# Optimization experiments

Measured on AMD Instinct MI355X. Metric: run time of the kernel, lower is better.

## Reference

```python
import jax, jax.numpy as jnp
import numpy as np

B = 2
C = 256          # hidden_dim / d_model
NH = 8           # attention heads
NL = 4           # feature levels
NP = 4           # sampling points per head per level
DH = C // NH
FF = 1024
NLAYERS = 6
SHAPES = [(64, 64), (32, 32), (16, 16), (8, 8)]
CIN = 256
OUT_CH = 2
IMG = 256


def setup_inputs() -> dict:
    key = jax.random.key(0)
    ks = iter(jax.random.split(key, 64))

    def nrm(shape, s=0.02):
        return jax.random.normal(next(ks), shape, jnp.float32) * s

    inp = {}
    for i, (h, w) in enumerate(SHAPES):
        inp[f"f{i}"] = jax.random.normal(next(ks), (B, CIN, h, w), jnp.float32)
    # input_proj: 1x1 conv + GroupNorm per level
    inp["proj_w"] = nrm((NL, C, CIN))
    inp["proj_b"] = jnp.zeros((NL, C), jnp.float32)
    inp["gn_w"] = jnp.ones((NL, C), jnp.float32)
    inp["gn_b"] = jnp.zeros((NL, C), jnp.float32)
    inp["level_embed"] = nrm((NL, C), 1.0)
    # 6 encoder layers (stacked params)
    inp["so_w"] = nrm((NLAYERS, NH * NL * NP * 2, C))   # sampling offsets
    inp["so_b"] = nrm((NLAYERS, NH * NL * NP * 2), 0.1)
    inp["aw_w"] = nrm((NLAYERS, NH * NL * NP, C))       # attention weights
    inp["aw_b"] = jnp.zeros((NLAYERS, NH * NL * NP), jnp.float32)
    inp["vp_w"] = nrm((NLAYERS, C, C))                   # value proj
    inp["vp_b"] = jnp.zeros((NLAYERS, C), jnp.float32)
    inp["op_w"] = nrm((NLAYERS, C, C))                   # output proj
    inp["op_b"] = jnp.zeros((NLAYERS, C), jnp.float32)
    inp["n1_w"] = jnp.ones((NLAYERS, C), jnp.float32)
    inp["n1_b"] = jnp.zeros((NLAYERS, C), jnp.float32)
    inp["l1_w"] = nrm((NLAYERS, FF, C))
    inp["l1_b"] = jnp.zeros((NLAYERS, FF), jnp.float32)
    inp["l2_w"] = nrm((NLAYERS, C, FF))
    inp["l2_b"] = jnp.zeros((NLAYERS, C), jnp.float32)
    inp["n2_w"] = jnp.ones((NLAYERS, C), jnp.float32)
    inp["n2_b"] = jnp.zeros((NLAYERS, C), jnp.float32)
    # classifier head convs
    inp["c1_w"] = nrm((64, C, 3, 3))
    inp["c1_b"] = jnp.zeros((64,), jnp.float32)
    inp["c2_w"] = nrm((OUT_CH, 64, 3, 3))
    inp["c2_b"] = jnp.zeros((OUT_CH,), jnp.float32)
    return inp


def group_norm(x, w, b, groups=32, eps=1e-5):
    Bq, Cc, H, W = x.shape
    xg = x.reshape(Bq, groups, Cc // groups, H, W)
    mu = xg.mean((2, 3, 4), keepdims=True)
    var = xg.var((2, 3, 4), keepdims=True)
    xg = (xg - mu) * jax.lax.rsqrt(var + eps)
    return xg.reshape(Bq, Cc, H, W) * w[None, :, None, None] + b[None, :, None, None]


def layer_norm(x, w, b, eps=1e-5):
    mu = x.mean(-1, keepdims=True)
    var = x.var(-1, keepdims=True)
    return (x - mu) * jax.lax.rsqrt(var + eps) * w + b


def pos_embed_sine(h, w, num_feats=C // 2):
    # PositionEmbeddingSine(normalize=True), mask all-False -> cumsum of ones
    eps = 1e-6
    scale = 2.0 * np.pi
    y = (jnp.arange(1, h + 1, dtype=jnp.float32) / (h + eps)) * scale
    x = (jnp.arange(1, w + 1, dtype=jnp.float32) / (w + eps)) * scale
    dim_t = 10000.0 ** (2.0 * (jnp.arange(num_feats) // 2).astype(jnp.float32) / num_feats)

    def enc(v):
        p = v[:, None] / dim_t  # [n, num_feats]
        return jnp.stack([jnp.sin(p[:, 0::2]), jnp.cos(p[:, 1::2])], -1).reshape(v.shape[0], num_feats)

    pe_y = enc(y)  # [h, 128]
    pe_x = enc(x)  # [w, 128]
    pos = jnp.concatenate([
        jnp.broadcast_to(pe_y[:, None, :], (h, w, num_feats)),
        jnp.broadcast_to(pe_x[None, :, :], (h, w, num_feats)),
    ], -1)  # [h, w, C], channels = (y, x)
    return pos.reshape(h * w, C)


def reference_points(shapes):
    pts = []
    for h, w in shapes:
        ry = (jnp.arange(h, dtype=jnp.float32) + 0.5) / h
        rx = (jnp.arange(w, dtype=jnp.float32) + 0.5) / w
        gy, gx = jnp.meshgrid(ry, rx, indexing='ij')
        pts.append(jnp.stack([gx, gy], -1).reshape(-1, 2))
    return jnp.concatenate(pts, 0)  # [Lq, 2] (x, y)


def bilinear_sample(v, x, y, Hl, Wl):
    # v: [B, NH, S, DH]; x, y: [B, Lq, NH, NP] pixel coords (align_corners=False, zero padding)
    x0 = jnp.floor(x); y0 = jnp.floor(y)
    fx = x - x0; fy = y - y0
    out = 0.0
    for dx, dy, wgt in ((0, 0, (1 - fx) * (1 - fy)), (1, 0, fx * (1 - fy)),
                        (0, 1, (1 - fx) * fy), (1, 1, fx * fy)):
        xi = x0 + dx; yi = y0 + dy
        valid = ((xi >= 0) & (xi < Wl) & (yi >= 0) & (yi < Hl)).astype(v.dtype)
        idx = (jnp.clip(yi, 0, Wl and Hl - 1) * Wl + jnp.clip(xi, 0, Wl - 1)).astype(jnp.int32)
        idx = (jnp.clip(yi, 0, Hl - 1) * Wl + jnp.clip(xi, 0, Wl - 1)).astype(jnp.int32)
        idxh = idx.transpose(0, 2, 1, 3).reshape(idx.shape[0], NH, -1)  # [B,NH,Lq*NP]
        g = jnp.take_along_axis(v, idxh[..., None], axis=2)             # [B,NH,Lq*NP,DH]
        w_ = (wgt * valid).transpose(0, 2, 1, 3).reshape(idx.shape[0], NH, -1, 1)
        out = out + g * w_
    return out  # [B, NH, Lq*NP, DH]


def ms_deform_attn(query, value_in, ref, starts,
                   so_w, so_b, aw_w, aw_b, vp_w, vp_b, op_w, op_b):
    Bq, Lq, _ = query.shape
    value = value_in @ vp_w.T + vp_b                                  # [B, Lin, C]
    value = value.reshape(Bq, -1, NH, DH).transpose(0, 2, 1, 3)       # [B, NH, Lin, DH]
    off = (query @ so_w.T + so_b).reshape(Bq, Lq, NH, NL, NP, 2)
    aw = (query @ aw_w.T + aw_b).reshape(Bq, Lq, NH, NL * NP)
    aw = jax.nn.softmax(aw, -1).reshape(Bq, Lq, NH, NL, NP)
    norm = jnp.array([[w, h] for (h, w) in SHAPES], jnp.float32)       # [NL, 2] (x, y)
    # sampling locations: ref (same across levels, valid_ratios=1) + normalized offsets
    loc = ref[None, :, None, None, None, :] + off / norm[None, None, None, :, None, :]
    out = jnp.zeros((Bq, NH, Lq, DH), jnp.float32)
    for l, (Hl, Wl) in enumerate(SHAPES):
        vl = jax.lax.dynamic_slice_in_dim(value, starts[l], Hl * Wl, axis=2)
        x = loc[:, :, :, l, :, 0] * Wl - 0.5
        y = loc[:, :, :, l, :, 1] * Hl - 0.5
        samp = bilinear_sample(vl, x, y, Hl, Wl).reshape(Bq, NH, Lq, NP, DH)
        out = out + jnp.einsum('bhqp,bhqpd->bhqd', aw[:, :, :, l].transpose(0, 2, 1, 3), samp)
    out = out.transpose(0, 2, 1, 3).reshape(Bq, Lq, C)
    return out @ op_w.T + op_b


def conv3x3(x, w, b):
    y = jax.lax.conv_general_dilated(x, w, (1, 1), ((1, 1), (1, 1)),
                                     dimension_numbers=('NCHW', 'OIHW', 'NCHW'))
    return y + b[None, :, None, None]


def reference(f0, f1, f2, f3, proj_w, proj_b, gn_w, gn_b, level_embed,
              so_w, so_b, aw_w, aw_b, vp_w, vp_b, op_w, op_b,
              n1_w, n1_b, l1_w, l1_b, l2_w, l2_b, n2_w, n2_b,
              c1_w, c1_b, c2_w, c2_b):
    feats = [f0, f1, f2, f3]
    srcs, poss = [], []
    for l, (h, w) in enumerate(SHAPES):
        x = jnp.einsum('oc,bchw->bohw', proj_w[l], feats[l]) + proj_b[l][None, :, None, None]
        x = group_norm(x, gn_w[l], gn_b[l])
        srcs.append(x.reshape(B, C, h * w).transpose(0, 2, 1))   # [B, HW, C]
        poss.append(pos_embed_sine(h, w) + level_embed[l])        # [HW, C]
    src = jnp.concatenate(srcs, 1)       # [B, Lq, C]
    pos = jnp.concatenate(poss, 0)       # [Lq, C]
    ref = reference_points(SHAPES)
    starts = np.cumsum([0] + [h * w for h, w in SHAPES])[:-1].tolist()
    x = src
    for i in range(NLAYERS):  # dropout=0 (eval mode)
        q = x + pos[None]
        a = ms_deform_attn(q, x, ref, starts,
                           so_w[i], so_b[i], aw_w[i], aw_b[i],
                           vp_w[i], vp_b[i], op_w[i], op_b[i])
        x = layer_norm(x + a, n1_w[i], n1_b[i])
        ff = jax.nn.relu(x @ l1_w[i].T + l1_b[i]) @ l2_w[i].T + l2_b[i]
        x = layer_norm(x + ff, n2_w[i], n2_b[i])
    h0, w0 = SHAPES[0]
    layer0 = x[:, :h0 * w0].reshape(B, h0, w0, C).transpose(0, 3, 1, 2)
    y = jax.nn.relu(conv3x3(layer0, c1_w, c1_b))
    y = conv3x3(y, c2_w, c2_b)
    return jax.image.resize(y, (B, OUT_CH, IMG, IMG), method='bilinear')
```

## Files before the change

### kernel.cpp

```cpp
#include <hip/hip_runtime.h>
#include <hip/hip_bf16.h>
#include <math.h>

#define LQ 5440
#define CDIM 256
#define BATCH 2
#define FFDIM 1024

typedef __attribute__((ext_vector_type(8))) short bf16x8;
typedef __attribute__((ext_vector_type(4))) float f32x4;

typedef __attribute__((address_space(1))) void* gas1_t;
typedef __attribute__((address_space(3))) void* las3_t;

__device__ __forceinline__ void async16(const void* g, void* l) {
  __builtin_amdgcn_global_load_lds((gas1_t)g, (las3_t)l, 16, 0, 0);
}

#define WAIT_VM5() asm volatile("s_waitcnt vmcnt(5)" ::: "memory")
#define WAIT_VM4() asm volatile("s_waitcnt vmcnt(4)" ::: "memory")
#define WAIT_VM3() asm volatile("s_waitcnt vmcnt(3)" ::: "memory")
#define WAIT_VM2() asm volatile("s_waitcnt vmcnt(2)" ::: "memory")
#define WAIT_VM0() asm volatile("s_waitcnt vmcnt(0)" ::: "memory")

// ... 52 lines not shown
  const int ksub = (lane >> 4) * 8;
  int cur = 0, nxt = 2;
  for (int t = 0; t < nt; ++t) {
    if (t == nt - 1) WAIT_VM0(); else WAIT_VM4();
    __builtin_amdgcn_s_barrier();
    asm volatile("" ::: "memory");
    bf16x8 af[4], bfv[4];
#pragma unroll
    for (int mi = 0; mi < 4; ++mi)
      af[mi] = *(const bf16x8*)&As[cur][(wr * 64 + mi * 16 + fr) * 32 + ksub];
#pragma unroll
    for (int nj = 0; nj < 4; ++nj)
      bfv[nj] = *(const bf16x8*)&Bs[cur][(wc * 64 + nj * 16 + fr) * 32 + ksub];
    if (t + 2 < nt) {
      const int ko = (t + 2) * 32;
      async16(ga0 + ko, &As[nxt][lo0]);
      async16(ga1 + ko, &As[nxt][lo1]);
      async16(gb0 + ko, &Bs[nxt][lo0]);
      async16(gb1 + ko, &Bs[nxt][lo1]);
    }
#pragma unroll
    for (int mi = 0; mi < 4; ++mi)
#pragma unroll
      for (int nj = 0; nj < 4; ++nj)
        acc[mi][nj] = __builtin_amdgcn_mfma_f32_16x16x32_bf16(af[mi], bfv[nj],
                                                              acc[mi][nj], 0, 0, 0);
    cur = (cur == 2) ? 0 : cur + 1;
    nxt = (nxt == 2) ? 0 : nxt + 1;
  }

  const int cc = lane & 15;
  const int rbase = (lane >> 4) * 4;
  float bcol[4];
#pragma unroll
  for (int nj = 0; nj < 4; ++nj) bcol[nj] = bias[bn + wc * 64 + nj * 16 + cc];
#pragma unroll
  for (int mi = 0; mi < 4; ++mi)
#pragma unroll
    for (int nj = 0; nj < 4; ++nj) {
      int col = bn + wc * 64 + nj * 16 + cc;
#pragma unroll
      for (int r = 0; r < 4; ++r) {
        int row = bm + wr * 64 + mi * 16 + rbase + r;
        size_t oaddr = (size_t)obase +
                       (row < mrows ? (size_t)row * N
                                    : (size_t)obstride + (size_t)(row - mrows) * N) +
                       col;
        x[oaddr] = acc[mi][nj][r] + bcol[nj];
      }
    }
}

template <bool RELU, bool OUT_F32, bool OUT_B16>
__device__ __forceinline__ void gemm64_body(
    const __hip_bfloat16* __restrict__ A, const __hip_bfloat16* __restrict__ Wt,
    const float* __restrict__ bias, float* __restrict__ C,
    __hip_bfloat16* __restrict__ Cb, int bm, int bn, int N, int K,
    __hip_bfloat16 (*As)[64 * 32], __hip_bfloat16 (*Bs)[128 * 32]) {
  const int tid = threadIdx.x;
  const int lane = tid & 63, wv = tid >> 6;
  const int srow = tid >> 2, scol = (tid & 3) * 8;
  const int loA = srow * 32 + scol;
  const int loB1 = (64 + srow) * 32 + scol;
  const __hip_bfloat16* ga = A + (size_t)(bm + srow) * K + scol;
  const __hip_bfloat16* gb0 = Wt + (size_t)(bn + srow) * K + scol;
  const __hip_bfloat16* gb1 = Wt + (size_t)(bn + 64 + srow) * K + scol;
  const int nt = K >> 5;
  async16(ga, &As[0][loA]);
  async16(gb0, &Bs[0][loA]);
  async16(gb1, &Bs[0][loB1]);
  async16(ga + 32, &As[1][loA]);
  async16(gb0 + 32, &Bs[1][loA]);
  async16(gb1 + 32, &Bs[1][loB1]);

  f32x4 acc[4][2] = {};
  const int fr = lane & 15, ksub = (lane >> 4) * 8;
  int cur = 0, nxt = 2;
  for (int t = 0; t < nt; ++t) {
    if (t == nt - 1) WAIT_VM0(); else WAIT_VM3();
    __builtin_amdgcn_s_barrier();
    asm volatile("" ::: "memory");
    bf16x8 af[4], bfv[2];
#pragma unroll
    for (int mi = 0; mi < 4; ++mi)
      af[mi] = *(const bf16x8*)&As[cur][(mi * 16 + fr) * 32 + ksub];
#pragma unroll
    for (int nj = 0; nj < 2; ++nj)
      bfv[nj] = *(const bf16x8*)&Bs[cur][(wv * 32 + nj * 16 + fr) * 32 + ksub];
    if (t + 2 < nt) {
      const int ko = (t + 2) * 32;
      async16(ga + ko, &As[nxt][loA]);
      async16(gb0 + ko, &Bs[nxt][loA]);
      async16(gb1 + ko, &Bs[nxt][loB1]);
    }
#pragma unroll
    for (int mi = 0; mi < 4; ++mi)
#pragma unroll
      for (int nj = 0; nj < 2; ++nj)
        acc[mi][nj] = __builtin_amdgcn_mfma_f32_16x16x32_bf16(af[mi], bfv[nj],
                                                              acc[mi][nj], 0, 0, 0);
    cur = (cur == 2) ? 0 : cur + 1;
    nxt = (nxt == 2) ? 0 : nxt + 1;
  }
  const int cc = lane & 15;
  const int rbase = (lane >> 4) * 4;
#pragma unroll
  for (int nj = 0; nj < 2; ++nj) {
    int col = bn + wv * 32 + nj * 16 + cc;
    float bb = bias[col];
#pragma unroll
    for (int mi = 0; mi < 4; ++mi)
#pragma unroll
      for (int r = 0; r < 4; ++r) {
        int row = bm + mi * 16 + rbase + r;
        float v = acc[mi][nj][r] + bb;
        if (RELU) v = fmaxf(v, 0.f);
        if (OUT_F32) C[(size_t)row * N + col] = v;
        if (OUT_B16) Cb[(size_t)row * N + col] = __float2bfloat16(v);
      }
  }
}

__global__ __launch_bounds__(256, 4) void gemm_dual_kernel(
    const __hip_bfloat16* __restrict__ xb, const __hip_bfloat16* __restrict__ vw,
    const float* __restrict__ vb, __hip_bfloat16* __restrict__ valb,
    const __hip_bfloat16* __restrict__ qb, const __hip_bfloat16* __restrict__ sowa,
    const float* __restrict__ sbias, float* __restrict__ comb) {
  __shared__ __hip_bfloat16 As[3][64 * 32];
  __shared__ __hip_bfloat16 Bs[3][128 * 32];
  if (blockIdx.x < 340) {
    int i = blockIdx.x;
    gemm64_body<false, false, true>(xb, vw, vb, nullptr, valb, (i >> 1) * 64,
                                    (i & 1) * 128, 256, 256, As, Bs);
  } else {
    int j = blockIdx.x - 340;
    gemm64_body<false, true, false>(qb, sowa, sbias, comb, nullptr, (j / 3) * 64,
                                    (j % 3) * 128, 384, 256, As, Bs);
  }
}

__global__ __launch_bounds__(256, 4) void ffn1_kernel(
    const __hip_bfloat16* __restrict__ xb, const __hip_bfloat16* __restrict__ w1,
    const float* __restrict__ b1, __hip_bfloat16* __restrict__ ff1b) {
  __shared__ __hip_bfloat16 As[3][64 * 32];
  __shared__ __hip_bfloat16 Bs[3][128 * 32];
  int i = blockIdx.x;
  gemm64_body<true, false, true>(xb, w1, b1, nullptr, ff1b, (i >> 3) * 64,
                                 (i & 7) * 128, 1024, 256, As, Bs);
}

template <bool EMIT_Q>
__global__ __launch_bounds__(256, 2) void gemm_ln_kernel(
    const __hip_bfloat16* __restrict__ A, const __hip_bfloat16* __restrict__ Wt,
    const float* __restrict__ bias, float* __restrict__ x,
    __hip_bfloat16* __restrict__ xb, __hip_bfloat16* __restrict__ qb,
    const float* __restrict__ pos, const float* __restrict__ lnw,
    const float* __restrict__ lnb, int K) {
  __shared__ __hip_bfloat16 As[3][32 * 32];
  __shared__ __hip_bfloat16 Bs[3][256 * 32];
  __shared__ float sred[4][32], ssred[4][32];
  const int tid = threadIdx.x;
  const int bm = blockIdx.x * 32;
  const int lane = tid & 63, wv = tid >> 6;
  const int srow = tid >> 2;
  const int arow = srow & 31;
  const int scol = (tid & 3) * 8;
  const int loA = arow * 32 + scol;
  const __hip_bfloat16* ga = A + (size_t)(bm + arow) * K + scol;
  const __hip_bfloat16* gb = Wt + (size_t)srow * K + scol;

  const int nt = K >> 5;
  auto stage = [&](int t, int buf) {
    const int ko = t * 32;
    async16(ga + ko, &As[buf][loA]);
#pragma unroll
    for (int i = 0; i < 4; ++i)
      async16(gb + (size_t)(64 * i) * K + ko, &Bs[buf][(64 * i + srow) * 32 + scol]);
  };
  stage(0, 0);
  stage(1, 1);

  f32x4 acc[2][4] = {};
  const int fr = lane & 15;
  const int ksub = (lane >> 4) * 8;

  int cur = 0, nxt = 2;
  for (int t = 0; t < nt; ++t) {
    if (t == nt - 1) WAIT_VM0(); else WAIT_VM5();
    __builtin_amdgcn_s_barrier();
    asm volatile("" ::: "memory");
    bf16x8 af[2], bfv[4];
#pragma unroll
    for (int mi = 0; mi < 2; ++mi)
      af[mi] = *(const bf16x8*)&As[cur][(mi * 16 + fr) * 32 + ksub];
#pragma unroll
    for (int nj = 0; nj < 4; ++nj)
      bfv[nj] = *(const bf16x8*)&Bs[cur][(wv * 64 + nj * 16 + fr) * 32 + ksub];
    if (t + 2 < nt) stage(t + 2, nxt);
#pragma unroll
    for (int mi = 0; mi < 2; ++mi)
#pragma unroll
      for (int nj = 0; nj < 4; ++nj)
        acc[mi][nj] = __builtin_amdgcn_mfma_f32_16x16x32_bf16(af[mi], bfv[nj],
                                                              acc[mi][nj], 0, 0, 0);
    cur = (cur == 2) ? 0 : cur + 1;
    nxt = (nxt == 2) ? 0 : nxt + 1;
  }

  const int cc = lane & 15;
  const int rbase = (lane >> 4) * 4;
  float bcol[4], wcol[4], bncol[4];
#pragma unroll
  for (int nj = 0; nj < 4; ++nj) {
    int col = wv * 64 + nj * 16 + cc;
    bcol[nj] = bias[col];
    wcol[nj] = lnw[col];
    bncol[nj] = lnb[col];
  }
#pragma unroll
  for (int mi = 0; mi < 2; ++mi)
#pragma unroll
    for (int r = 0; r < 4; ++r) {
      int grow = bm + mi * 16 + rbase + r;
#pragma unroll
      for (int nj = 0; nj < 4; ++nj) {
        int col = wv * 64 + nj * 16 + cc;
        acc[mi][nj][r] += bcol[nj] + x[(size_t)grow * 256 + col];
      }
    }
#pragma unroll
  for (int mi = 0; mi < 2; ++mi)
#pragma unroll
    for (int r = 0; r < 4; ++r) {
      float s = 0.f, ssq = 0.f;
#pragma unroll
      for (int nj = 0; nj < 4; ++nj) {
        float v = acc[mi][nj][r];
        s += v;
        ssq += v * v;
      }
#pragma unroll
      for (int m = 1; m < 16; m <<= 1) {
        s += __shfl_xor(s, m);
        ssq += __shfl_xor(ssq, m);
      }
      if (cc == 0) {
        int row = mi * 16 + rbase + r;
        sred[wv][row] = s;
        ssred[wv][row] = ssq;
      }
    }
  __syncthreads();
#pragma unroll
  for (int mi = 0; mi < 2; ++mi)
#pragma unroll
    for (int r = 0; r < 4; ++r) {
      int row = mi * 16 + rbase + r;
      int grow = bm + row;
      float s = sred[0][row] + sred[1][row] + sred[2][row] + sred[3][row];
      float ssq = ssred[0][row] + ssred[1][row] + ssred[2][row] + ssred[3][row];
      float mu = s * (1.0f / 256.0f);
      float var = ssq * (1.0f / 256.0f) - mu * mu;
      float rsig = rsqrtf(var + 1e-5f);
      int tokp = grow >= LQ ? grow - LQ : grow;
#pragma unroll
      for (int nj = 0; nj < 4; ++nj) {
        int col = wv * 64 + nj * 16 + cc;
        float xn = (acc[mi][nj][r] - mu) * rsig * wcol[nj] + bncol[nj];
        x[(size_t)grow * 256 + col] = xn;
        xb[(size_t)grow * 256 + col] = __float2bfloat16(xn);
        if (EMIT_Q)
          qb[(size_t)grow * 256 + col] =
              __float2bfloat16(xn + pos[(size_t)tokp * 256 + col]);
      }
    }
}

__global__ __launch_bounds__(256, 4) void conv1_mfma_kernel(
    const __hip_bfloat16* __restrict__ xb, const __hip_bfloat16* __restrict__ wc1,
    const float* __restrict__ bias, const __hip_bfloat16* __restrict__ zerob,
    __hip_bfloat16* __restrict__ c1o) {
  __shared__ __hip_bfloat16 As[3][64 * 32];
  __shared__ __hip_bfloat16 Bs[3][64 * 32];
  const int tid = threadIdx.x;
  const int b = blockIdx.x >> 6;
  const int pm = (blockIdx.x & 63) * 64;
  const int lane = tid & 63, wave = tid >> 6;
  const int sr = tid >> 2;
  const int sc = (tid & 3) * 8;
  const int lo = sr * 32 + sc;
  f32x4 acc[4] = {};
  const int fr = lane & 15, ksub = (lane >> 4) * 8;

  auto stage = [&](int kt, int buf) {
    int tap = kt >> 3;
    int kk = (kt & 7) * 32;
    int dy = tap / 3 - 1, dx = tap % 3 - 1;
    int hw = pm + sr;
    int y = (hw >> 6) + dy, x = (hw & 63) + dx;
    bool ok = (y >= 0 && y < 64 && x >= 0 && x < 64);
    const __hip_bfloat16* s =
        xb + ((size_t)(b * LQ) + y * 64 + x) * 256 + kk + sc;
    const __hip_bfloat16* wsrc = wc1 + (size_t)sr * 2304 + tap * 256 + kk + sc;
    async16(ok ? s : zerob, &As[buf][lo]);
    async16(wsrc, &Bs[buf][lo]);
  };
  stage(0, 0);
  stage(1, 1);
  int cur = 0, nxt = 2;
  for (int kt = 0; kt < 72; ++kt) {
    if (kt == 71) WAIT_VM0(); else WAIT_VM2();
    __builtin_amdgcn_s_barrier();
    asm volatile("" ::: "memory");
    bf16x8 af;
    bf16x8 bfv[4];
    af = *(const bf16x8*)&As[cur][(wave * 16 + fr) * 32 + ksub];
#pragma unroll
    for (int nj = 0; nj < 4; ++nj)
      bfv[nj] = *(const bf16x8*)&Bs[cur][(nj * 16 + fr) * 32 + ksub];
    if (kt + 2 < 72) stage(kt + 2, nxt);
#pragma unroll
    for (int nj = 0; nj < 4; ++nj)
      acc[nj] = __builtin_amdgcn_mfma_f32_16x16x32_bf16(af, bfv[nj], acc[nj], 0, 0, 0);
    cur = (cur == 2) ? 0 : cur + 1;
    nxt = (nxt == 2) ? 0 : nxt + 1;
  }
  const int cc = lane & 15;
  const int rbase = (lane >> 4) * 4;
#pragma unroll
  for (int nj = 0; nj < 4; ++nj) {
    int col = nj * 16 + cc;
    float bb = bias[col];
#pragma unroll
    for (int r = 0; r < 4; ++r) {
      int row = wave * 16 + rbase + r;
      float v = fmaxf(acc[nj][r] + bb, 0.f);
      c1o[(size_t)(b * 4096 + pm + row) * 64 + col] = __float2bfloat16(v);
    }
  }
}

__global__ void f2b_multi_kernel(const float* __restrict__ p0, const float* __restrict__ p1,
                                 const float* __restrict__ p2, const float* __restrict__ p3,
                                 const float* __restrict__ p4,
                                 __hip_bfloat16* __restrict__ o0, __hip_bfloat16* __restrict__ o1,
                                 __hip_bfloat16* __restrict__ o2, __hip_bfloat16* __restrict__ o3,
                                 __hip_bfloat16* __restrict__ o4) {
  int i = blockIdx.x * 256 + threadIdx.x;
  if (i >= 1048576) return;
  const float* in;
  __hip_bfloat16* out;
  int j;
  if (i < 65536)       { in = p0; out = o0; j = i; }
  else if (i < 163840) { in = p1; out = o1; j = i - 65536; }
  else if (i < 262144) { in = p2; out = o2; j = i - 163840; }
  else if (i < 655360) { in = p3; out = o3; j = i - 262144; }
  else                 { in = p4; out = o4; j = i - 655360; }
  float4 v = ((const float4*)in)[j];
  union { ushort4 u; __hip_bfloat16 h[4]; } p;
  p.h[0] = __float2bfloat16(v.x);
  p.h[1] = __float2bfloat16(v.y);
  p.h[2] = __float2bfloat16(v.z);
  p.h[3] = __float2bfloat16(v.w);
  ((ushort4*)out)[j] = p.u;
}

__global__ void sowa_prep_kernel(const float* __restrict__ so_w,
                                 const float* __restrict__ aw_w,
                                 const float* __restrict__ so_b,
                                 const float* __restrict__ aw_b,
                                 __hip_bfloat16* __restrict__ out,
                                 float* __restrict__ bias_out) {
  int i = blockIdx.x * 256 + threadIdx.x;
  if (i < 6 * 384 * 256) {
    int il = i / (384 * 256);
    int rem = i - il * 384 * 256;
    int n = rem >> 8, k = rem & 255;
    float v = (n < 256) ? so_w[(size_t)il * 65536 + n * 256 + k]
                        : aw_w[(size_t)il * 32768 + (n - 256) * 256 + k];
    out[i] = __float2bfloat16(v);
  } else if (i < 6 * 384 * 256 + 6 * 384) {
    int j = i - 6 * 384 * 256;
    int il = j / 384, n = j % 384;
    bias_out[j] = (n < 256) ? so_b[il * 256 + n] : aw_b[il * 128 + n - 256];
  }
}

__global__ void wc1_prep_kernel(const float* __restrict__ w,
                                __hip_bfloat16* __restrict__ out) {
  int i = blockIdx.x * 256 + threadIdx.x;
  if (i >= 64 * 2304) return;
  int oc = i / 2304, r = i % 2304;
  int tap = r >> 8, ic = r & 255;
  out[i] = __float2bfloat16(w[(size_t)oc * 2304 + ic * 9 + tap]);
}

__global__ __launch_bounds__(256) void transpose_f_kernel(
    const float* __restrict__ f0, const float* __restrict__ f1,
    const float* __restrict__ f2, const float* __restrict__ f3,
    __hip_bfloat16* __restrict__ ft) {
  __shared__ float tile[64][65];
  const int HWs[4] = {4096, 1024, 256, 64};
  const int STs[4] = {0, 4096, 5120, 5376};
  int chunk = blockIdx.x, c0 = blockIdx.y * 64, b = blockIdx.z;
  int l, row0;
  get_chunk(chunk, l, row0);
  const float* fin = (l == 0) ? f0 : (l == 1) ? f1 : (l == 2) ? f2 : f3;
  const int HW = HWs[l];
  int t = threadIdx.x;
  int cr = t >> 4, hc4 = (t & 15) * 4;
#pragma unroll
  for (int p = 0; p < 4; ++p) {
    int c = c0 + p * 16 + cr;
    float4 v = *(const float4*)&fin[(size_t)(b * 256 + c) * HW + row0 + hc4];
    tile[p * 16 + cr][hc4 + 0] = v.x;
    tile[p * 16 + cr][hc4 + 1] = v.y;
    tile[p * 16 + cr][hc4 + 2] = v.z;
    tile[p * 16 + cr][hc4 + 3] = v.w;
  }
  __syncthreads();
  size_t obase = (size_t)2 * STs[l] * 256 + ((size_t)b * HW + row0) * 256 + c0;
#pragma unroll
  for (int p = 0; p < 4; ++p) {
    int r = p * 16 + cr;
    union { ushort4 u; __hip_bfloat16 h[4]; } pk;
    pk.h[0] = __float2bfloat16(tile[hc4 + 0][r]);
    pk.h[1] = __float2bfloat16(tile[hc4 + 1][r]);
    pk.h[2] = __float2bfloat16(tile[hc4 + 2][r]);
    pk.h[3] = __float2bfloat16(tile[hc4 + 3][r]);
    *(ushort4*)&ft[obase + (size_t)r * 256 + hc4] = pk.u;
  }
}

__global__ __launch_bounds__(256) void gn_part_kernel(const float* __restrict__ x,
                                                      float2* __restrict__ part) {
  const int STs[4] = {0, 4096, 5120, 5376};
  int chunk = blockIdx.x, b = blockIdx.y;
  int l, row0;
  get_chunk(chunk, l, row0);
  size_t base = ((size_t)b * LQ + STs[l] + row0) * 256;
  int t = threadIdx.x;
  int col4 = t & 63, rb = t >> 6;
  float s = 0.f, ss = 0.f;
#pragma unroll 4
  for (int i = 0; i < 16; ++i) {
    int r = rb + i * 4;
    float4 v = *(const float4*)&x[base + (size_t)r * 256 + col4 * 4];
    s += v.x + v.y + v.z + v.w;
    ss += v.x * v.x + v.y * v.y + v.z * v.z + v.w * v.w;
  }
  __shared__ float sA[256], sB[256];
  sA[t] = s;
  sB[t] = ss;
  __syncthreads();
  if (t < 64) {
    s = sA[t] + sA[t + 64] + sA[t + 128] + sA[t + 192];
    ss = sB[t] + sB[t + 64] + sB[t + 128] + sB[t + 192];
    sA[t] = s;
    sB[t] = ss;
  }
  __syncthreads();
  if (t < 32)
    part[((size_t)b * 85 + chunk) * 32 + t] =
        make_float2(sA[2 * t] + sA[2 * t + 1], sB[2 * t] + sB[2 * t + 1]);
}

__global__ void gn_finalize_kernel(const float2* __restrict__ part,
                                   float2* __restrict__ stats) {
  int t = threadIdx.x;
  int b = t >> 7, rem = t & 127, l = rem >> 5, g = rem & 31;
  const int cnt_[4] = {64, 16, 4, 1};
  const int cb_[4] = {0, 64, 80, 84};
  const int HWs[4] = {4096, 1024, 256, 64};
  float s = 0.f, ss = 0.f;
  for (int i = 0; i < cnt_[l]; ++i) {
    float2 v = part[((size_t)b * 85 + cb_[l] + i) * 32 + g];
    s += v.x;
    ss += v.y;
  }
  float n = (float)(HWs[l] * 8);
  float mu = s / n;
  float var = ss / n - mu * mu;
  stats[(b * 4 + l) * 32 + g] = make_float2(mu, rsqrtf(var + 1e-5f));
}

__device__ __forceinline__ void get_level(int t, int& l, int& hw, int& Hl, int& Wl) {
  if (t < 4096)      { l = 0; hw = t;        Hl = 64; Wl = 64; }
  else if (t < 5120) { l = 1; hw = t - 4096; Hl = 32; Wl = 32; }
  else if (t < 5376) { l = 2; hw = t - 5120; Hl = 16; Wl = 16; }
  else               { l = 3; hw = t - 5376; Hl = 8;  Wl = 8;  }
}

__global__ void gn_apply_kernel(float* __restrict__ x, __hip_bfloat16* __restrict__ xb,
                                __hip_bfloat16* __restrict__ qb,
                                const float* __restrict__ pos,
                                const float2* __restrict__ stats,
                                const float* __restrict__ gw, const float* __restrict__ gb) {
  int idx = blockIdx.x * 256 + threadIdx.x;
  if (idx >= BATCH * LQ * CDIM) return;
  int c = idx & 255;
  int tok = idx >> 8;
  int b = tok / LQ, t = tok % LQ;
  int l, hw, Hl, Wl;
  get_level(t, l, hw, Hl, Wl);
  float2 st = stats[(b * 4 + l) * 32 + (c >> 3)];
  float v = (x[idx] - st.x) * st.y * gw[l * CDIM + c] + gb[l * CDIM + c];
  x[idx] = v;
  xb[idx] = __float2bfloat16(v);
  qb[idx] = __float2bfloat16(v + pos[t * 256 + c]);
}

__global__ void pos_ref_kernel(const float* __restrict__ level_embed,
                               float* __restrict__ pos, float* __restrict__ ref) {
  int idx = blockIdx.x * 256 + threadIdx.x;
  if (idx >= LQ * CDIM) return;
  int t = idx >> 8, c = idx & 255;
  int l, hw, Hl, Wl;
  get_level(t, l, hw, Hl, Wl);
  int y = hw / Wl, xx = hw % Wl;
  const float twopi = 6.28318530717958647692f;
  float v; int cc;
  if (c < 128) { v = (float)(y + 1) * twopi / ((float)Hl + 1e-6f); cc = c; }
  else         { v = (float)(xx + 1) * twopi / ((float)Wl + 1e-6f); cc = c - 128; }
  int k = cc >> 1;
  float dim_t = expf((float)k * (logf(10000.0f) / 64.0f));
  float p = v / dim_t;
  float e = (cc & 1) ? cosf(p) : sinf(p);
  pos[idx] = e + level_embed[l * CDIM + c];
  if (c == 0) {
    ref[t * 2]     = ((float)xx + 0.5f) / (float)Wl;
    ref[t * 2 + 1] = ((float)y + 0.5f) / (float)Hl;
  }
}

__global__ __launch_bounds__(256) void deform_attn_kernel(
    const __hip_bfloat16* __restrict__ value, const float* __restrict__ comb,
    const float* __restrict__ ref, __hip_bfloat16* __restrict__ out) {
  const int Wl_[4] = {64, 32, 16, 8};
  const int st_[4] = {0, 4096, 5120, 5376};
  int gid = blockIdx.x * 64 + (threadIdx.x >> 2);
  int lane4 = threadIdx.x & 3;
  int h = gid & 7;
  int tok = gid >> 3;
  int b = tok / LQ;
  int qi = tok - b * LQ;

  const float4* awv = (const float4*)(comb + (size_t)tok * 384 + 256 + h * 16);
  float4 q0 = awv[0], q1 = awv[1], q2 = awv[2], q3 = awv[3];
  float logit[16] = {q0.x, q0.y, q0.z, q0.w, q1.x, q1.y, q1.z, q1.w,
                     q2.x, q2.y, q2.z, q2.w, q3.x, q3.y, q3.z, q3.w};
  float mx = -1e30f;
#pragma unroll
  for (int i = 0; i < 16; ++i) mx = fmaxf(mx, logit[i]);
  const float LOG2E = 1.4426950408889634f;
  float ssum = 0.f;
#pragma unroll
  for (int i = 0; i < 16; ++i) {
    logit[i] = exp2f((logit[i] - mx) * LOG2E);
    ssum += logit[i];
  }
  float inv = 1.0f / ssum;

  float rx = ref[qi * 2], ry = ref[qi * 2 + 1];
  const float4* offv = (const float4*)(comb + (size_t)tok * 384 + h * 32);
  float acc[8] = {};

#pragma unroll
  for (int l = 0; l < 4; ++l) {
    const int Wl = Wl_[l];
    const float fW = (float)Wl;
    const __hip_bfloat16* vbase =
        value + ((size_t)b * LQ + st_[l]) * CDIM + h * 32 + lane4 * 8;
    float bx = fmaf(rx, fW, -0.5f);
    float by = fmaf(ry, fW, -0.5f);
    float4 oa = offv[l * 2], ob = offv[l * 2 + 1];
    float oxs[4] = {oa.x, oa.z, ob.x, ob.z};
    float oys[4] = {oa.y, oa.w, ob.y, ob.w};
#pragma unroll
    for (int p = 0; p < 4; ++p) {
      float px = bx + oxs[p], py = by + oys[p];
      float wgt = logit[l * 4 + p] * inv;
      float fpx = floorf(px), fpy = floorf(py);
      int x0 = (int)fpx, y0 = (int)fpy;
      float fx = px - fpx, fy = py - fpy;
      float wx0 = (x0 >= 0 && x0 < Wl) ? (1.f - fx) : 0.f;
      float wx1 = (x0 >= -1 && x0 < Wl - 1) ? fx : 0.f;
      float wy0 = (y0 >= 0 && y0 < Wl) ? (wgt * (1.f - fy)) : 0.f;
      float wy1 = (y0 >= -1 && y0 < Wl - 1) ? (wgt * fy) : 0.f;
      int xc0 = min(max(x0, 0), Wl - 1);
      int xc1 = min(max(x0 + 1, 0), Wl - 1);
      int yc0 = min(max(y0, 0), Wl - 1);
      int yc1 = min(max(y0 + 1, 0), Wl - 1);
      const __hip_bfloat16* r0 = vbase + (size_t)(yc0 * Wl) * CDIM;
      const __hip_bfloat16* r1 = vbase + (size_t)(yc1 * Wl) * CDIM;
      bf16x8 u00 = *(const bf16x8*)(r0 + (size_t)xc0 * CDIM);
      bf16x8 u01 = *(const bf16x8*)(r0 + (size_t)xc1 * CDIM);
      bf16x8 u10 = *(const bf16x8*)(r1 + (size_t)xc0 * CDIM);
      bf16x8 u11 = *(const bf16x8*)(r1 + (size_t)xc1 * CDIM);
      float w00 = wy0 * wx0, w01 = wy0 * wx1, w10 = wy1 * wx0, w11 = wy1 * wx1;
#pragma unroll
      for (int k = 0; k < 8; ++k) {
        float v00 = __uint_as_float((unsigned)(unsigned short)u00[k] << 16);
        float v01 = __uint_as_float((unsigned)(unsigned short)u01[k] << 16);
        float v10 = __uint_as_float((unsigned)(unsigned short)u10[k] << 16);
        float v11 = __uint_as_float((unsigned)(unsigned short)u11[k] << 16);
        acc[k] = fmaf(w00, v00, acc[k]);
        acc[k] = fmaf(w01, v01, acc[k]);
        acc[k] = fmaf(w10, v10, acc[k]);
        acc[k] = fmaf(w11, v11, acc[k]);
      }
    }
  }
  union { bf16x8 u; __hip_bfloat16 hh[8]; } pk;
#pragma unroll
  for (int k = 0; k < 8; ++k) pk.hh[k] = __float2bfloat16(acc[k]);
  *(bf16x8*)(out + (size_t)tok * CDIM + h * 32 + lane4 * 8) = pk.u;
}

__global__ __launch_bounds__(256) void conv2_part_kernel(
    const __hip_bfloat16* __restrict__ c1o, const float* __restrict__ w,
    float* __restrict__ part) {
  int pix = blockIdx.x * 256 + threadIdx.x;
  int tap = blockIdx.y, b = blockIdx.z;
  int y = pix >> 6, x = pix & 63;
  int dy = tap / 3 - 1, dx = tap % 3 - 1;
  int yy = y + dy, xx = x + dx;
  bool ok = (yy >= 0 && yy < 64 && xx >= 0 && xx < 64);
  float a0 = 0.f, a1 = 0.f;
  if (ok) {
    const __hip_bfloat16* row = c1o + (size_t)(b * 4096 + yy * 64 + xx) * 64;
#pragma unroll
    for (int ic4 = 0; ic4 < 16; ++ic4) {
      ushort4 u = *(const ushort4*)(row + ic4 * 4);
      float f0 = __uint_as_float((unsigned)u.x << 16);
      float f1 = __uint_as_float((unsigned)u.y << 16);
      float f2 = __uint_as_float((unsigned)u.z << 16);
      float f3 = __uint_as_float((unsigned)u.w << 16);
      int ic = ic4 * 4;
      a0 = fmaf(w[(ic + 0) * 9 + tap], f0, a0);
      a0 = fmaf(w[(ic + 1) * 9 + tap], f1, a0);
      a0 = fmaf(w[(ic + 2) * 9 + tap], f2, a0);
      a0 = fmaf(w[(ic + 3) * 9 + tap], f3, a0);
      a1 = fmaf(w[576 + (ic + 0) * 9 + tap], f0, a1);
      a1 = fmaf(w[576 + (ic + 1) * 9 + tap], f1, a1);
      a1 = fmaf(w[576 + (ic + 2) * 9 + tap], f2, a1);
      a1 = fmaf(w[576 + (ic + 3) * 9 + tap], f3, a1);
    }
  }
  float2 o = make_float2(a0, a1);
  *(float2*)&part[((size_t)(tap * BATCH + b) * 4096 + pix) * 2] = o;
}

__global__ void conv2_reduce_kernel(const float* __restrict__ part,
                                    const float* __restrict__ bias,
                                    float* __restrict__ out) {
  int i = blockIdx.x * 256 + threadIdx.x;
  if (i >= BATCH * 4096) return;
  int b = i >> 12, pix = i & 4095;
  float s0 = bias[0], s1 = bias[1];
#pragma unroll
  for (int tap = 0; tap < 9; ++tap) {
    float2 v = *(const float2*)&part[((size_t)(tap * BATCH + b) * 4096 + pix) * 2];
    s0 += v.x; s1 += v.y;
  }
  *(float2*)&out[(size_t)i * 2] = make_float2(s0, s1);
}

__global__ void upsample_kernel(const float* __restrict__ in, float* __restrict__ out) {
  int idx = blockIdx.x * 256 + threadIdx.x;
  if (idx >= BATCH * 2 * 256 * 256) return;
  int X = idx & 255, Y = (idx >> 8) & 255, p = idx >> 16;
  int b = p >> 1, oc = p & 1;
  float tx = ((float)X + 0.5f) * 0.25f - 0.5f;
  float ty = ((float)Y + 0.5f) * 0.25f - 0.5f;
  float fxf = floorf(tx), fyf = floorf(ty);
  int x0 = (int)fxf, y0 = (int)fyf;
  float fx = tx - fxf, fy = ty - fyf;
  int x0c = min(max(x0, 0), 63), x1c = min(max(x0 + 1, 0), 63);
  int y0c = min(max(y0, 0), 63), y1c = min(max(y0 + 1, 0), 63);
  const float* ip = in + (size_t)b * 4096 * 2 + oc;
  float v = (1.f - fy) * ((1.f - fx) * ip[(y0c * 64 + x0c) * 2] + fx * ip[(y0c * 64 + x1c) * 2]) +
            fy * ((1.f - fx) * ip[(y1c * 64 + x0c) * 2] + fx * ip[(y1c * 64 + x1c) * 2]);
  out[idx] = v;
}

extern "C" void kernel_launch(void* const* d_in, const int* in_sizes, int n_in,
                              void* d_out, int out_size, void* d_ws, size_t ws_size,
                              hipStream_t stream) {
  const float* f[4] = {(const float*)d_in[0], (const float*)d_in[1],
                       (const float*)d_in[2], (const float*)d_in[3]};
  const float* proj_w = (const float*)d_in[4];
  const float* proj_b = (const float*)d_in[5];
  const float* gn_w = (const float*)d_in[6];
  const float* gn_b = (const float*)d_in[7];
  const float* level_embed = (const float*)d_in[8];
  const float* so_w = (const float*)d_in[9];
  const float* so_b = (const float*)d_in[10];
  const float* aw_w = (const float*)d_in[11];
  const float* aw_b = (const float*)d_in[12];
  const float* vp_w = (const float*)d_in[13];
  const float* vp_b = (const float*)d_in[14];
  const float* op_w = (const float*)d_in[15];
  const float* op_b = (const float*)d_in[16];
  const float* n1_w = (const float*)d_in[17];
  const float* n1_b = (const float*)d_in[18];
  const float* l1_w = (const float*)d_in[19];
  const float* l1_b = (const float*)d_in[20];
  const float* l2_w = (const float*)d_in[21];
  const float* l2_b = (const float*)d_in[22];
  const float* n2_w = (const float*)d_in[23];
  const float* n2_b = (const float*)d_in[24];
  const float* c1_w = (const float*)d_in[25];
  const float* c1_b = (const float*)d_in[26];
  const float* c2_w = (const float*)d_in[27];
  const float* c2_b = (const float*)d_in[28];
  (void)in_sizes; (void)n_in; (void)out_size; (void)ws_size;

  float* ws = (float*)d_ws;
  const size_t TOK = (size_t)BATCH * LQ * CDIM;
  size_t o = 0;
  float* x = ws + o;     o += TOK;
  float* comb = ws + o;  o += (size_t)BATCH * LQ * 384;
  float* pos = ws + o;   o += (size_t)LQ * CDIM;
  float* refb = ws + o;  o += 11008;
  float2* stats = (float2*)(ws + o); o += 512;
  float* zerof = ws + o; o += 256;
  float* sowa_bias = ws + o; o += 2304;
  float2* gnpart = (float2*)(ws + o); o += 11008;
  __hip_bfloat16* xb = (__hip_bfloat16*)(ws + o);    o += TOK / 2;
  __hip_bfloat16* qb = (__hip_bfloat16*)(ws + o);    o += TOK / 2;
  __hip_bfloat16* valb = (__hip_bfloat16*)(ws + o);  o += TOK / 2;
  __hip_bfloat16* attnb = (__hip_bfloat16*)(ws + o); o += TOK / 2;
  __hip_bfloat16* ftb = (__hip_bfloat16*)(ws + o);   o += TOK / 2;
  __hip_bfloat16* ff1b = (__hip_bfloat16*)(ws + o);  o += (size_t)BATCH * LQ * FFDIM / 2;
  __hip_bfloat16* sowa_wb = (__hip_bfloat16*)(ws + o); o += 294912;
  __hip_bfloat16* vp_wb = (__hip_bfloat16*)(ws + o); o += 196608;
  __hip_bfloat16* op_wb = (__hip_bfloat16*)(ws + o); o += 196608;
  __hip_bfloat16* l1_wb = (__hip_bfloat16*)(ws + o); o += 786432;
  __hip_bfloat16* l2_wb = (__hip_bfloat16*)(ws + o); o += 786432;
  __hip_bfloat16* proj_wb = (__hip_bfloat16*)(ws + o); o += 131072;
  __hip_bfloat16* wc1b = (__hip_bfloat16*)(ws + o);  o += 73728;
  __hip_bfloat16* c1ob = ff1b;
  float* part2 = (float*)(ff1b + 524288);
  float* c2o = part2 + 147456;

  hipMemsetAsync(zerof, 0, 1024, stream);
  sowa_prep_kernel<<<(6 * 384 * 256 + 6 * 384 + 255) / 256, 256, 0, stream>>>(
      so_w, aw_w, so_b, aw_b, sowa_wb, sowa_bias);
  wc1_prep_kernel<<<(147456 + 255) / 256, 256, 0, stream>>>(c1_w, wc1b);
  f2b_multi_kernel<<<(1048576 + 255) / 256, 256, 0, stream>>>(
      proj_w, vp_w, op_w, l1_w, l2_w, proj_wb, vp_wb, op_wb, l1_wb, l2_wb);

  transpose_f_kernel<<<dim3(85, 4, BATCH), 256, 0, stream>>>(f[0], f[1], f[2], f[3],
                                                             ftb);
  input_proj_kernel<<<170, 256, 0, stream>>>(ftb, proj_wb, proj_b, x);
  pos_ref_kernel<<<(LQ * CDIM + 255) / 256, 256, 0, stream>>>(level_embed, pos, refb);
  gn_part_kernel<<<dim3(85, BATCH), 256, 0, stream>>>(x, gnpart);
  gn_finalize_kernel<<<1, 256, 0, stream>>>(gnpart, stats);
  {
    int n = BATCH * LQ * CDIM;
    gn_apply_kernel<<<(n + 255) / 256, 256, 0, stream>>>(x, xb, qb, pos, stats,
                                                         gn_w, gn_b);
  }

  for (int i = 0; i < 6; ++i) {
    const __hip_bfloat16* sowa = sowa_wb + (size_t)i * 98304;
    const __hip_bfloat16* vw = vp_wb + (size_t)i * 65536;
    const __hip_bfloat16* ow = op_wb + (size_t)i * 65536;
    const __hip_bfloat16* w1 = l1_wb + (size_t)i * 262144;
    const __hip_bfloat16* w2 = l2_wb + (size_t)i * 262144;
    const float* vb = vp_b + (size_t)i * CDIM;
    const float* ob = op_b + (size_t)i * CDIM;
    const float* b1 = l1_b + (size_t)i * FFDIM;
    const float* b2 = l2_b + (size_t)i * CDIM;

    gemm_dual_kernel<<<850, 256, 0, stream>>>(xb, vw, vb, valb, qb, sowa,
                                              sowa_bias + i * 384, comb);
    deform_attn_kernel<<<BATCH * LQ * 8 / 64, 256, 0, stream>>>(valb, comb, refb,
                                                                attnb);
    gemm_ln_kernel<false><<<340, 256, 0, stream>>>(
        attnb, ow, ob, x, xb, nullptr, nullptr,
        n1_w + (size_t)i * CDIM, n1_b + (size_t)i * CDIM, CDIM);
    ffn1_kernel<<<1360, 256, 0, stream>>>(xb, w1, b1, ff1b);
    gemm_ln_kernel<true><<<340, 256, 0, stream>>>(
        ff1b, w2, b2, x, xb, qb, pos,
        n2_w + (size_t)i * CDIM, n2_b + (size_t)i * CDIM, FFDIM);
  }

  conv1_mfma_kernel<<<128, 256, 0, stream>>>(xb, wc1b, c1_b,
                                             (const __hip_bfloat16*)zerof, c1ob);
  conv2_part_kernel<<<dim3(16, 9, BATCH), 256, 0, stream>>>(c1ob, c2_w, part2);
  conv2_reduce_kernel<<<(BATCH * 4096 + 255) / 256, 256, 0, stream>>>(part2, c2_b,
                                                                      c2o);
  {
    int n = BATCH * 2 * 256 * 256;
    upsample_kernel<<<(n + 255) / 256, 256, 0, stream>>>(c2o, (float*)d_out);
  }
}
```

Measured before the change: 621.0 us.

## Merge prep kernels, fold GN finalize and conv2 reduce, drop fp32 residual

```diff
diff --git a/kernel.cpp b/kernel.cpp
--- a/kernel.cpp
+++ b/kernel.cpp
@@ -228,10 +228,9 @@
 template <bool EMIT_Q>
 __global__ __launch_bounds__(256, 2) void gemm_ln_kernel(
     const __hip_bfloat16* __restrict__ A, const __hip_bfloat16* __restrict__ Wt,
-    const float* __restrict__ bias, float* __restrict__ x,
-    __hip_bfloat16* __restrict__ xb, __hip_bfloat16* __restrict__ qb,
-    const float* __restrict__ pos, const float* __restrict__ lnw,
-    const float* __restrict__ lnb, int K) {
+    const float* __restrict__ bias, __hip_bfloat16* xb,
+    __hip_bfloat16* __restrict__ qb, const float* __restrict__ pos,
+    const float* __restrict__ lnw, const float* __restrict__ lnb, int K) {
   __shared__ __hip_bfloat16 As[3][32 * 32];
   __shared__ __hip_bfloat16 Bs[3][256 * 32];
   __shared__ float sred[4][32], ssred[4][32];
@@ -301,7 +300,7 @@
 #pragma unroll
       for (int nj = 0; nj < 4; ++nj) {
         int col = wv * 64 + nj * 16 + cc;
-        acc[mi][nj][r] += bcol[nj] + x[(size_t)grow * 256 + col];
+        acc[mi][nj][r] += bcol[nj] + __bfloat162float(xb[(size_t)grow * 256 + col]);
       }
     }
 #pragma unroll
@@ -343,7 +342,6 @@
       for (int nj = 0; nj < 4; ++nj) {
         int col = wv * 64 + nj * 16 + cc;
         float xn = (acc[mi][nj][r] - mu) * rsig * wcol[nj] + bncol[nj];
-        x[(size_t)grow * 256 + col] = xn;
         xb[(size_t)grow * 256 + col] = __float2bfloat16(xn);
         if (EMIT_Q)
           qb[(size_t)grow * 256 + col] =
@@ -416,59 +414,54 @@
   }
 }
 
-__global__ void f2b_multi_kernel(const float* __restrict__ p0, const float* __restrict__ p1,
-                                 const float* __restrict__ p2, const float* __restrict__ p3,
-                                 const float* __restrict__ p4,
-                                 __hip_bfloat16* __restrict__ o0, __hip_bfloat16* __restrict__ o1,
-                                 __hip_bfloat16* __restrict__ o2, __hip_bfloat16* __restrict__ o3,
-                                 __hip_bfloat16* __restrict__ o4) {
+__global__ void prep_all_kernel(
+    const float* __restrict__ proj_w, const float* __restrict__ vp_w,
+    const float* __restrict__ op_w, const float* __restrict__ l1_w,
+    const float* __restrict__ l2_w, const float* __restrict__ so_w,
+    const float* __restrict__ aw_w, const float* __restrict__ so_b,
+    const float* __restrict__ aw_b, const float* __restrict__ c1_w,
+    __hip_bfloat16* __restrict__ proj_wb, __hip_bfloat16* __restrict__ vp_wb,
+    __hip_bfloat16* __restrict__ op_wb, __hip_bfloat16* __restrict__ l1_wb,
+    __hip_bfloat16* __restrict__ l2_wb, __hip_bfloat16* __restrict__ sowa_wb,
+    float* __restrict__ sowa_bias, __hip_bfloat16* __restrict__ wc1b,
+    float* __restrict__ zerof) {
   int i = blockIdx.x * 256 + threadIdx.x;
-  if (i >= 1048576) return;
-  const float* in;
-  __hip_bfloat16* out;
-  int j;
-  if (i < 65536)       { in = p0; out = o0; j = i; }
-  else if (i < 163840) { in = p1; out = o1; j = i - 65536; }
-  else if (i < 262144) { in = p2; out = o2; j = i - 163840; }
-  else if (i < 655360) { in = p3; out = o3; j = i - 262144; }
-  else                 { in = p4; out = o4; j = i - 655360; }
-  float4 v = ((const float4*)in)[j];
-  union { ushort4 u; __hip_bfloat16 h[4]; } p;
-  p.h[0] = __float2bfloat16(v.x);
-  p.h[1] = __float2bfloat16(v.y);
-  p.h[2] = __float2bfloat16(v.z);
-  p.h[3] = __float2bfloat16(v.w);
-  ((ushort4*)out)[j] = p.u;
-}
-
-__global__ void sowa_prep_kernel(const float* __restrict__ so_w,
-                                 const float* __restrict__ aw_w,
-                                 const float* __restrict__ so_b,
-                                 const float* __restrict__ aw_b,
-                                 __hip_bfloat16* __restrict__ out,
-                                 float* __restrict__ bias_out) {
-  int i = blockIdx.x * 256 + threadIdx.x;
-  if (i < 6 * 384 * 256) {
-    int il = i / (384 * 256);
-    int rem = i - il * 384 * 256;
+  if (i < 1048576) {
+    const float* in;
+    __hip_bfloat16* out;
+    int j;
+    if (i < 65536)       { in = proj_w; out = proj_wb; j = i; }
+    else if (i < 163840) { in = vp_w;   out = vp_wb;   j = i - 65536; }
+    else if (i < 262144) { in = op_w;   out = op_wb;   j = i - 163840; }
+    else if (i < 655360) { in = l1_w;   out = l1_wb;   j = i - 262144; }
+    else                 { in = l2_w;   out = l2_wb;   j = i - 655360; }
+    float4 v = ((const float4*)in)[j];
+    union { ushort4 u; __hip_bfloat16 h[4]; } p;
+    p.h[0] = __float2bfloat16(v.x);
+    p.h[1] = __float2bfloat16(v.y);
+    p.h[2] = __float2bfloat16(v.z);
+    p.h[3] = __float2bfloat16(v.w);
+    ((ushort4*)out)[j] = p.u;
+  } else if (i < 1638400) {
+    int j = i - 1048576;
+    int il = j / (384 * 256);
+    int rem = j - il * 384 * 256;
     int n = rem >> 8, k = rem & 255;
     float v = (n < 256) ? so_w[(size_t)il * 65536 + n * 256 + k]
                         : aw_w[(size_t)il * 32768 + (n - 256) * 256 + k];
-    out[i] = __float2bfloat16(v);
-  } else if (i < 6 * 384 * 256 + 6 * 384) {
-    int j = i - 6 * 384 * 256;
+    sowa_wb[j] = __float2bfloat16(v);
+  } else if (i < 1640704) {
+    int j = i - 1638400;
     int il = j / 384, n = j % 384;
-    bias_out[j] = (n < 256) ? so_b[il * 256 + n] : aw_b[il * 128 + n - 256];
-  }
-}
-
-__global__ void wc1_prep_kernel(const float* __restrict__ w,
-                                __hip_bfloat16* __restrict__ out) {
-  int i = blockIdx.x * 256 + threadIdx.x;
-  if (i >= 64 * 2304) return;
-  int oc = i / 2304, r = i % 2304;
-  int tap = r >> 8, ic = r & 255;
-  out[i] = __float2bfloat16(w[(size_t)oc * 2304 + ic * 9 + tap]);
+    sowa_bias[j] = (n < 256) ? so_b[il * 256 + n] : aw_b[il * 128 + n - 256];
+  } else if (i < 1788160) {
+    int j = i - 1640704;
+    int oc = j / 2304, r = j % 2304;
+    int tap = r >> 8, ic = r & 255;
+    wc1b[j] = __float2bfloat16(c1_w[(size_t)oc * 2304 + ic * 9 + tap]);
+  } else if (i < 1788416) {
+    zerof[i - 1788160] = 0.f;
+  }
 }
 
 __global__ __launch_bounds__(256) void transpose_f_kernel(
@@ -541,25 +534,6 @@
         make_float2(sA[2 * t] + sA[2 * t + 1], sB[2 * t] + sB[2 * t + 1]);
 }
 
-__global__ void gn_finalize_kernel(const float2* __restrict__ part,
-                                   float2* __restrict__ stats) {
-  int t = threadIdx.x;
-  int b = t >> 7, rem = t & 127, l = rem >> 5, g = rem & 31;
-  const int cnt_[4] = {64, 16, 4, 1};
-  const int cb_[4] = {0, 64, 80, 84};
-  const int HWs[4] = {4096, 1024, 256, 64};
-  float s = 0.f, ss = 0.f;
-  for (int i = 0; i < cnt_[l]; ++i) {
-    float2 v = part[((size_t)b * 85 + cb_[l] + i) * 32 + g];
-    s += v.x;
-    ss += v.y;
-  }
-  float n = (float)(HWs[l] * 8);
-  float mu = s / n;
-  float var = ss / n - mu * mu;
-  stats[(b * 4 + l) * 32 + g] = make_float2(mu, rsqrtf(var + 1e-5f));
-}
-
 __device__ __forceinline__ void get_level(int t, int& l, int& hw, int& Hl, int& Wl) {
   if (t < 4096)      { l = 0; hw = t;        Hl = 64; Wl = 64; }
   else if (t < 5120) { l = 1; hw = t - 4096; Hl = 32; Wl = 32; }
@@ -567,29 +541,29 @@
   else               { l = 3; hw = t - 5376; Hl = 8;  Wl = 8;  }
 }
 
-__global__ void gn_apply_kernel(float* __restrict__ x, __hip_bfloat16* __restrict__ xb,
-                                __hip_bfloat16* __restrict__ qb,
-                                const float* __restrict__ pos,
-                                const float2* __restrict__ stats,
-                                const float* __restrict__ gw, const float* __restrict__ gb) {
+__global__ void pos_ref_fin_kernel(const float* __restrict__ level_embed,
+                                   float* __restrict__ pos, float* __restrict__ ref,
+                                   const float2* __restrict__ part,
+                                   float2* __restrict__ stats) {
+  if (blockIdx.x == 5440) {
+    int t = threadIdx.x;
+    int b = t >> 7, rem = t & 127, l = rem >> 5, g = rem & 31;
+    const int cnt_[4] = {64, 16, 4, 1};
+    const int cb_[4] = {0, 64, 80, 84};
+    const int HWs[4] = {4096, 1024, 256, 64};
+    float s = 0.f, ss = 0.f;
+    for (int i = 0; i < cnt_[l]; ++i) {
+      float2 v = part[((size_t)b * 85 + cb_[l] + i) * 32 + g];
+      s += v.x;
+      ss += v.y;
+    }
+    float n = (float)(HWs[l] * 8);
+    float mu = s / n;
+    float var = ss / n - mu * mu;
+    stats[(b * 4 + l) * 32 + g] = make_float2(mu, rsqrtf(var + 1e-5f));
+    return;
+  }
   int idx = blockIdx.x * 256 + threadIdx.x;
-  if (idx >= BATCH * LQ * CDIM) return;
-  int c = idx & 255;
-  int tok = idx >> 8;
-  int b = tok / LQ, t = tok % LQ;
-  int l, hw, Hl, Wl;
-  get_level(t, l, hw, Hl, Wl);
-  float2 st = stats[(b * 4 + l) * 32 + (c >> 3)];
-  float v = (x[idx] - st.x) * st.y * gw[l * CDIM + c] + gb[l * CDIM + c];
-  x[idx] = v;
-  xb[idx] = __float2bfloat16(v);
-  qb[idx] = __float2bfloat16(v + pos[t * 256 + c]);
-}
-
-__global__ void pos_ref_kernel(const float* __restrict__ level_embed,
-                               float* __restrict__ pos, float* __restrict__ ref) {
-  int idx = blockIdx.x * 256 + threadIdx.x;
-  if (idx >= LQ * CDIM) return;
   int t = idx >> 8, c = idx & 255;
   int l, hw, Hl, Wl;
   get_level(t, l, hw, Hl, Wl);
@@ -607,6 +581,25 @@
     ref[t * 2]     = ((float)xx + 0.5f) / (float)Wl;
     ref[t * 2 + 1] = ((float)y + 0.5f) / (float)Hl;
   }
+}
+
+__global__ void gn_apply_kernel(const float* __restrict__ x,
+                                __hip_bfloat16* __restrict__ xb,
+                                __hip_bfloat16* __restrict__ qb,
+                                const float* __restrict__ pos,
+                                const float2* __restrict__ stats,
+                                const float* __restrict__ gw, const float* __restrict__ gb) {
+  int idx = blockIdx.x * 256 + threadIdx.x;
+  if (idx >= BATCH * LQ * CDIM) return;
+  int c = idx & 255;
+  int tok = idx >> 8;
+  int b = tok / LQ, t = tok % LQ;
+  int l, hw, Hl, Wl;
+  get_level(t, l, hw, Hl, Wl);
+  float2 st = stats[(b * 4 + l) * 32 + (c >> 3)];
+  float v = (x[idx] - st.x) * st.y * gw[l * CDIM + c] + gb[l * CDIM + c];
+  xb[idx] = __float2bfloat16(v);
+  qb[idx] = __float2bfloat16(v + pos[t * 256 + c]);
 }
 
 __global__ __launch_bounds__(256) void deform_attn_kernel(
@@ -727,26 +720,12 @@
   *(float2*)&part[((size_t)(tap * BATCH + b) * 4096 + pix) * 2] = o;
 }
 
-__global__ void conv2_reduce_kernel(const float* __restrict__ part,
-                                    const float* __restrict__ bias,
-                                    float* __restrict__ out) {
-  int i = blockIdx.x * 256 + threadIdx.x;
-  if (i >= BATCH * 4096) return;
-  int b = i >> 12, pix = i & 4095;
-  float s0 = bias[0], s1 = bias[1];
-#pragma unroll
-  for (int tap = 0; tap < 9; ++tap) {
-    float2 v = *(const float2*)&part[((size_t)(tap * BATCH + b) * 4096 + pix) * 2];
-    s0 += v.x; s1 += v.y;
-  }
-  *(float2*)&out[(size_t)i * 2] = make_float2(s0, s1);
-}
-
-__global__ void upsample_kernel(const float* __restrict__ in, float* __restrict__ out) {
+__global__ void upsample2_kernel(const float* __restrict__ part,
+                                 const float* __restrict__ bias,
+                                 float* __restrict__ out) {
   int idx = blockIdx.x * 256 + threadIdx.x;
-  if (idx >= BATCH * 2 * 256 * 256) return;
-  int X = idx & 255, Y = (idx >> 8) & 255, p = idx >> 16;
-  int b = p >> 1, oc = p & 1;
+  if (idx >= BATCH * 65536) return;
+  int X = idx & 255, Y = (idx >> 8) & 255, b = idx >> 16;
   float tx = ((float)X + 0.5f) * 0.25f - 0.5f;
   float ty = ((float)Y + 0.5f) * 0.25f - 0.5f;
   float fxf = floorf(tx), fyf = floorf(ty);
@@ -754,10 +733,30 @@
   float fx = tx - fxf, fy = ty - fyf;
   int x0c = min(max(x0, 0), 63), x1c = min(max(x0 + 1, 0), 63);
   int y0c = min(max(y0, 0), 63), y1c = min(max(y0 + 1, 0), 63);
-  const float* ip = in + (size_t)b * 4096 * 2 + oc;
-  float v = (1.f - fy) * ((1.f - fx) * ip[(y0c * 64 + x0c) * 2] + fx * ip[(y0c * 64 + x1c) * 2]) +
-            fy * ((1.f - fx) * ip[(y1c * 64 + x0c) * 2] + fx * ip[(y1c * 64 + x1c) * 2]);
-  out[idx] = v;
+  int p00 = y0c * 64 + x0c, p01 = y0c * 64 + x1c;
+  int p10 = y1c * 64 + x0c, p11 = y1c * 64 + x1c;
+  float c00x = 0.f, c00y = 0.f, c01x = 0.f, c01y = 0.f;
+  float c10x = 0.f, c10y = 0.f, c11x = 0.f, c11y = 0.f;
+#pragma unroll
+  for (int tap = 0; tap < 9; ++tap) {
+    const float* pp = part + ((size_t)(tap * BATCH + b) * 4096) * 2;
+    float2 v00 = *(const float2*)&pp[p00 * 2];
+    float2 v01 = *(const float2*)&pp[p01 * 2];
+    float2 v10 = *(const float2*)&pp[p10 * 2];
+    float2 v11 = *(const float2*)&pp[p11 * 2];
+    c00x += v00.x; c00y += v00.y;
+    c01x += v01.x; c01y += v01.y;
+    c10x += v10.x; c10y += v10.y;
+    c11x += v11.x; c11y += v11.y;
+  }
+  float b0 = bias[0], b1 = bias[1];
+  float w00 = (1.f - fy) * (1.f - fx), w01 = (1.f - fy) * fx;
+  float w10 = fy * (1.f - fx), w11 = fy * fx;
+  float o0 = w00 * (c00x + b0) + w01 * (c01x + b0) + w10 * (c10x + b0) + w11 * (c11x + b0);
+  float o1 = w00 * (c00y + b1) + w01 * (c01y + b1) + w10 * (c10y + b1) + w11 * (c11y + b1);
+  size_t obase = (size_t)b * 2 * 65536 + (Y << 8) + X;
+  out[obase] = o0;
+  out[obase + 65536] = o1;
 }
 
 extern "C" void kernel_launch(void* const* d_in, const int* in_sizes, int n_in,
@@ -818,21 +817,16 @@
   __hip_bfloat16* wc1b = (__hip_bfloat16*)(ws + o);  o += 73728;
   __hip_bfloat16* c1ob = ff1b;
   float* part2 = (float*)(ff1b + 524288);
-  float* c2o = part2 + 147456;
-
-  hipMemsetAsync(zerof, 0, 1024, stream);
-  sowa_prep_kernel<<<(6 * 384 * 256 + 6 * 384 + 255) / 256, 256, 0, stream>>>(
-      so_w, aw_w, so_b, aw_b, sowa_wb, sowa_bias);
-  wc1_prep_kernel<<<(147456 + 255) / 256, 256, 0, stream>>>(c1_w, wc1b);
-  f2b_multi_kernel<<<(1048576 + 255) / 256, 256, 0, stream>>>(
-      proj_w, vp_w, op_w, l1_w, l2_w, proj_wb, vp_wb, op_wb, l1_wb, l2_wb);
+
+  prep_all_kernel<<<(1788416 + 255) / 256, 256, 0, stream>>>(
+      proj_w, vp_w, op_w, l1_w, l2_w, so_w, aw_w, so_b, aw_b, c1_w,
+      proj_wb, vp_wb, op_wb, l1_wb, l2_wb, sowa_wb, sowa_bias, wc1b, zerof);
 
   transpose_f_kernel<<<dim3(85, 4, BATCH), 256, 0, stream>>>(f[0], f[1], f[2], f[3],
                                                              ftb);
   input_proj_kernel<<<170, 256, 0, stream>>>(ftb, proj_wb, proj_b, x);
-  pos_ref_kernel<<<(LQ * CDIM + 255) / 256, 256, 0, stream>>>(level_embed, pos, refb);
   gn_part_kernel<<<dim3(85, BATCH), 256, 0, stream>>>(x, gnpart);
-  gn_finalize_kernel<<<1, 256, 0, stream>>>(gnpart, stats);
+  pos_ref_fin_kernel<<<5441, 256, 0, stream>>>(level_embed, pos, refb, gnpart, stats);
   {
     int n = BATCH * LQ * CDIM;
     gn_apply_kernel<<<(n + 255) / 256, 256, 0, stream>>>(x, xb, qb, pos, stats,
@@ -855,21 +849,17 @@
     deform_attn_kernel<<<BATCH * LQ * 8 / 64, 256, 0, stream>>>(valb, comb, refb,
                                                                 attnb);
     gemm_ln_kernel<false><<<340, 256, 0, stream>>>(
-        attnb, ow, ob, x, xb, nullptr, nullptr,
+        attnb, ow, ob, xb, nullptr, nullptr,
         n1_w + (size_t)i * CDIM, n1_b + (size_t)i * CDIM, CDIM);
     ffn1_kernel<<<1360, 256, 0, stream>>>(xb, w1, b1, ff1b);
     gemm_ln_kernel<true><<<340, 256, 0, stream>>>(
-        ff1b, w2, b2, x, xb, qb, pos,
+        ff1b, w2, b2, xb, qb, pos,
         n2_w + (size_t)i * CDIM, n2_b + (size_t)i * CDIM, FFDIM);
   }
 
   conv1_mfma_kernel<<<128, 256, 0, stream>>>(xb, wc1b, c1_b,
                                              (const __hip_bfloat16*)zerof, c1ob);
   conv2_part_kernel<<<dim3(16, 9, BATCH), 256, 0, stream>>>(c1ob, c2_w, part2);
-  conv2_reduce_kernel<<<(BATCH * 4096 + 255) / 256, 256, 0, stream>>>(part2, c2_b,
-                                                                      c2o);
-  {
-    int n = BATCH * 2 * 256 * 256;
-    upsample_kernel<<<(n + 255) / 256, 256, 0, stream>>>(c2o, (float*)d_out);
-  }
-}
+  upsample2_kernel<<<(BATCH * 65536 + 255) / 256, 256, 0, stream>>>(part2, c2_b,
+                                                                    (float*)d_out);
+}
```

After: 586.6 us. 1.06x faster.
